# Kernel tuning notes

Hardware: AMD Instinct MI355X
Metric: run time of the kernel (lower is better)

## Reference

```python
import jax, jax.numpy as jnp
import numpy as np

IN_F = 4096
OUT_F = 4096
BATCH = 1024

def setup_inputs() -> dict:
    key = jax.random.key(0)
    k = jax.random.split(key, 7)
    x = jax.random.normal(k[0], (BATCH, IN_F), dtype=jnp.float32)
    weight_mu = jax.random.normal(k[1], (OUT_F, IN_F), dtype=jnp.float32) * (1.0 / np.sqrt(IN_F))
    # torch init: uniform(-5,-3) for sigma params (raw values, used directly as std)
    weight_sigma = jax.random.uniform(k[2], (OUT_F, IN_F), dtype=jnp.float32, minval=-5.0, maxval=-3.0)
    bias_mu = jnp.zeros((OUT_F,), dtype=jnp.float32)
    bias_sigma = jax.random.uniform(k[3], (OUT_F,), dtype=jnp.float32, minval=-5.0, maxval=-3.0)
    eps_w = jax.random.normal(k[4], (OUT_F, IN_F), dtype=jnp.float32)
    eps_b = jax.random.normal(k[5], (OUT_F,), dtype=jnp.float32)
    return {"x": x, "weight_mu": weight_mu, "weight_sigma": weight_sigma,
            "bias_mu": bias_mu, "bias_sigma": bias_sigma,
            "eps_w": eps_w, "eps_b": eps_b}

def reference(x, weight_mu, weight_sigma, bias_mu, bias_sigma, eps_w, eps_b):
    # training-mode forward: reparameterized weight sample then dense matmul
    weight = weight_mu + eps_w * weight_sigma        # [out, in]
    bias = bias_mu + eps_b * bias_sigma              # [out]
    # F.linear(x, W, b) = x @ W.T + b
    return jnp.einsum('bi,oi->bo', x, weight) + bias
```

## Files before the change

### kernel.cpp

```cpp
#include <hip/hip_runtime.h>
#include <hip/hip_bf16.h>
#include <stdint.h>

#define M_BATCH 1024
#define N_OUT   4096
#define K_IN    4096

#define BM 128
#define BN 128
#define BK 64
#define KSPLIT 2
#define KPER  (K_IN / KSPLIT)
#define KITER (KPER / BK)

typedef __attribute__((ext_vector_type(8))) __bf16 bf16x8_t;
typedef __attribute__((ext_vector_type(4))) float f32x4_t;

__device__ __forceinline__ unsigned short f2bf_bits(float f) {
    union { __hip_bfloat16 h; unsigned short u; } cvt;
    cvt.h = __float2bfloat16(f);
    return cvt.u;
}

struct __align__(8) US4 { unsigned short x, y, z, w; };

__global__ __launch_bounds__(256) void prep_kernel(
    const float* __restrict__ x,
    const float* __restrict__ wmu,
    const float* __restrict__ wsig,
    const float* __restrict__ epsw,
    unsigned short* __restrict__ wb,
    unsigned short* __restrict__ xb,
    float4* __restrict__ czero)
{
    const size_t tid    = (size_t)blockIdx.x * blockDim.x + threadIdx.x;
    const size_t stride = (size_t)gridDim.x * blockDim.x;

    const size_t NW4 = (size_t)N_OUT * K_IN / 4;
    const float4* wmu4  = (const float4*)wmu;
    const float4* wsig4 = (const float4*)wsig;
    const float4* epsw4 = (const float4*)epsw;
    US4* wb4 = (US4*)wb;
    for (size_t i = tid; i < NW4; i += stride) {
        float4 m = wmu4[i], s = wsig4[i], e = epsw4[i];
        US4 o;
        o.x = f2bf_bits(fmaf(e.x, s.x, m.x));
        o.y = f2bf_bits(fmaf(e.y, s.y, m.y));
        o.z = f2bf_bits(fmaf(e.z, s.z, m.z));
        o.w = f2bf_bits(fmaf(e.w, s.w, m.w));
        wb4[i] = o;
    }

    const size_t NX4 = (size_t)M_BATCH * K_IN / 4;
    const float4* x4 = (const float4*)x;
    US4* xb4 = (US4*)xb;
    for (size_t i = tid; i < NX4; i += stride) {
        float4 v = x4[i];
        US4 o;
        o.x = f2bf_bits(v.x);
        o.y = f2bf_bits(v.y);
        o.z = f2bf_bits(v.z);
        o.w = f2bf_bits(v.w);
        xb4[i] = o;
    }

    const size_t NC4 = (size_t)M_BATCH * N_OUT / 4;
    const float4 z = {0.f, 0.f, 0.f, 0.f};
    for (size_t i = tid; i < NC4; i += stride) czero[i] = z;
}

__global__ __launch_bounds__(256, 2) void gemm_bt_kernel(
    const unsigned short* __restrict__ A,
    const unsigned short* __restrict__ B,
    const float* __restrict__ bmu,
    const float* __restrict__ bsig,
    const float* __restrict__ ebias,
    float* __restrict__ C)
{
    __shared__ unsigned short As[2 * BM * BK];
    __shared__ unsigned short Bs[2 * BN * BK];

    const int t     = threadIdx.x;
    const int bm0   = blockIdx.y * BM;
    const int bn0   = blockIdx.x * BN;
    const int kbase = blockIdx.z * KPER;
    const int lane  = t & 63;
    const int wave  = t >> 6;
    const int wrow  = (wave >> 1) * 64;
    const int wcol  = (wave & 1) * 64;
    const int lm    = lane & 15;
    const int quad  = lane >> 4;

    f32x4_t acc[4][4] = {};

    const int srow = t >> 3;
    const int jg   = (t & 7) ^ (srow & 7);
    const unsigned short* ag = A + (size_t)(bm0 + srow) * K_IN + kbase + jg * 8;
    const unsigned short* bg = B + (size_t)(bn0 + srow) * K_IN + kbase + jg * 8;
    char* asDst = (char*)As + t * 16;
    char* bsDst = (char*)Bs + t * 16;

    #pragma unroll
    for (int s = 0; s < 4; ++s) {
        __builtin_amdgcn_global_load_lds(
            (const __attribute__((address_space(1))) void*)(ag + (size_t)s * 32 * K_IN),
            (__attribute__((address_space(3))) void*)(asDst + s * 4096), 16, 0, 0);
        __builtin_amdgcn_global_load_lds(
            (const __attribute__((address_space(1))) void*)(bg + (size_t)s * 32 * K_IN),
            (__attribute__((address_space(3))) void*)(bsDst + s * 4096), 16, 0, 0);
    }

    for (int it = 0; it < KITER; ++it) {
        __syncthreads();

        if (it + 1 < KITER) {
            const int koff = (it + 1) * BK;
            const int nb   = ((it + 1) & 1) * 16384;
            #pragma unroll
            for (int s = 0; s < 4; ++s) {
                __builtin_amdgcn_global_load_lds(
                    (const __attribute__((address_space(1))) void*)(ag + (size_t)s * 32 * K_IN + koff),
                    (__attribute__((address_space(3))) void*)(asDst + nb + s * 4096), 16, 0, 0);
                __builtin_amdgcn_global_load_lds(
                    (const __attribute__((address_space(1))) void*)(bg + (size_t)s * 32 * K_IN + koff),
                    (__attribute__((address_space(3))) void*)(bsDst + nb + s * 4096), 16, 0, 0);
            }
        }

        const unsigned short* Ab = As + (it & 1) * 8192;
        const unsigned short* Bb = Bs + (it & 1) * 8192;

        #pragma unroll
        for (int kk = 0; kk < 2; ++kk) {
            const int pbase = kk * 4;
            bf16x8_t a_frag[4], b_frag[4];
            #pragma unroll
            for (int im = 0; im < 4; im++) {
                const int R = wrow + im * 16 + lm;
                const int p = (pbase + quad) ^ (lm & 7);
                a_frag[im] = *(const bf16x8_t*)(Ab + R * BK + p * 8);
            }
            #pragma unroll
            for (int jn = 0; jn < 4; jn++) {
                const int R = wcol + jn * 16 + lm;
                const int p = (pbase + quad) ^ (lm & 7);
                b_frag[jn] = *(const bf16x8_t*)(Bb + R * BK + p * 8);
            }
            #pragma unroll
            for (int im = 0; im < 4; im++)
                #pragma unroll
                for (int jn = 0; jn < 4; jn++)
                    acc[im][jn] = __builtin_amdgcn_mfma_f32_16x16x32_bf16(
                        a_frag[im], b_frag[jn], acc[im][jn], 0, 0, 0);
        }
    }

    #pragma unroll
    for (int jn = 0; jn < 4; jn++) {
        const int gn = bn0 + wcol + jn * 16 + lm;
        const float bias = (kbase == 0) ? (bmu[gn] + ebias[gn] * bsig[gn]) : 0.f;
        #pragma unroll
        for (int im = 0; im < 4; im++) {
            const int gm0 = bm0 + wrow + im * 16 + quad * 4;
            #pragma unroll
            for (int r = 0; r < 4; r++)
                atomicAdd(&C[(size_t)(gm0 + r) * N_OUT + gn], acc[im][jn][r] + bias);
        }
    }
}

__global__ __launch_bounds__(256) void naive_kernel(
    const float* __restrict__ x, const float* __restrict__ wmu,
    const float* __restrict__ wsig, const float* __restrict__ bmu,
    const float* __restrict__ bsig, const float* __restrict__ epsw,
    const float* __restrict__ epsb, float* __restrict__ out)
{
    const int o = blockIdx.x * blockDim.x + threadIdx.x;
    const int b = blockIdx.y;
    const float4* xr = (const float4*)(x + (size_t)b * K_IN);
    const float4* mr = (const float4*)(wmu + (size_t)o * K_IN);
    const float4* sr = (const float4*)(wsig + (size_t)o * K_IN);
    const float4* er = (const float4*)(epsw + (size_t)o * K_IN);
    float s = 0.f;
    for (int k = 0; k < K_IN / 4; k++) {
        float4 xv = xr[k], m = mr[k], sg = sr[k], e = er[k];
        s += xv.x * fmaf(e.x, sg.x, m.x);
        s += xv.y * fmaf(e.y, sg.y, m.y);
        s += xv.z * fmaf(e.z, sg.z, m.z);
        s += xv.w * fmaf(e.w, sg.w, m.w);
    }
    out[(size_t)b * N_OUT + o] = s + bmu[o] + epsb[o] * bsig[o];
}

extern "C" void kernel_launch(void* const* d_in, const int* in_sizes, int n_in,
                              void* d_out, int out_size, void* d_ws, size_t ws_size,
                              hipStream_t stream)
{
    const float* x    = (const float*)d_in[0];
    const float* wmu  = (const float*)d_in[1];
    const float* wsig = (const float*)d_in[2];
    const float* bmu  = (const float*)d_in[3];
    const float* bsig = (const float*)d_in[4];
    const float* epsw = (const float*)d_in[5];
    const float* epsb = (const float*)d_in[6];
    float* out = (float*)d_out;

    const size_t need = ((size_t)N_OUT * K_IN + (size_t)M_BATCH * K_IN) * sizeof(unsigned short);
    if (ws_size >= need) {
        unsigned short* wb = (unsigned short*)d_ws;
        unsigned short* xb = wb + (size_t)N_OUT * K_IN;
        prep_kernel<<<2048, 256, 0, stream>>>(x, wmu, wsig, epsw, wb, xb, (float4*)out);
        dim3 grid(N_OUT / BN, M_BATCH / BM, KSPLIT);
        gemm_bt_kernel<<<grid, 256, 0, stream>>>(xb, wb, bmu, bsig, epsb, out);
    } else {
        dim3 grid(N_OUT / 256, M_BATCH);
        naive_kernel<<<grid, 256, 0, stream>>>(x, wmu, wsig, bmu, bsig, epsw, epsb, out);
    }
}
```

Baseline: 281.1 us.

## Replace split-K atomics with in-block K-split reduction and unrolled prep

The split-K over two blocks with atomicAdd into a pre-zeroed output becomes a single 512-thread block whose two wave groups each handle half of K. The halves are reduced through LDS and written with plain stores plus bias. This removes the output zeroing pass and the global atomics. The prep kernel is also rewritten with a fixed grid, 4-way unrolled nontemporal loads and no grid-stride loop. LDS use doubles to 128KB per block, which likely limits occupancy to one block per CU despite the launch bound of 2.

Measured after the change: 242.7 us. 1.16x faster.

```diff
diff --git a/kernel.cpp b/kernel.cpp
--- a/kernel.cpp
+++ b/kernel.cpp
@@ -9,12 +9,12 @@
 #define BM 128
 #define BN 128
 #define BK 64
-#define KSPLIT 2
-#define KPER  (K_IN / KSPLIT)
+#define KPER  (K_IN / 2)
 #define KITER (KPER / BK)
 
 typedef __attribute__((ext_vector_type(8))) __bf16 bf16x8_t;
 typedef __attribute__((ext_vector_type(4))) float f32x4_t;
+typedef __attribute__((ext_vector_type(4))) float fvec4;
 
 __device__ __forceinline__ unsigned short f2bf_bits(float f) {
     union { __hip_bfloat16 h; unsigned short u; } cvt;
@@ -30,46 +30,44 @@
     const float* __restrict__ wsig,
     const float* __restrict__ epsw,
     unsigned short* __restrict__ wb,
-    unsigned short* __restrict__ xb,
-    float4* __restrict__ czero)
-{
-    const size_t tid    = (size_t)blockIdx.x * blockDim.x + threadIdx.x;
-    const size_t stride = (size_t)gridDim.x * blockDim.x;
-
-    const size_t NW4 = (size_t)N_OUT * K_IN / 4;
-    const float4* wmu4  = (const float4*)wmu;
-    const float4* wsig4 = (const float4*)wsig;
-    const float4* epsw4 = (const float4*)epsw;
+    unsigned short* __restrict__ xb)
+{
+    const size_t tid = (size_t)blockIdx.x * blockDim.x + threadIdx.x;
+    const size_t T   = (size_t)1048576;
+
+    const fvec4* wmu4  = (const fvec4*)wmu;
+    const fvec4* wsig4 = (const fvec4*)wsig;
+    const fvec4* epsw4 = (const fvec4*)epsw;
     US4* wb4 = (US4*)wb;
-    for (size_t i = tid; i < NW4; i += stride) {
-        float4 m = wmu4[i], s = wsig4[i], e = epsw4[i];
+
+    fvec4 m[4], s[4], e[4];
+    #pragma unroll
+    for (int r = 0; r < 4; ++r) {
+        const size_t i = tid + (size_t)r * T;
+        m[r] = __builtin_nontemporal_load(wmu4  + i);
+        s[r] = __builtin_nontemporal_load(wsig4 + i);
+        e[r] = __builtin_nontemporal_load(epsw4 + i);
+    }
+    #pragma unroll
+    for (int r = 0; r < 4; ++r) {
         US4 o;
-        o.x = f2bf_bits(fmaf(e.x, s.x, m.x));
-        o.y = f2bf_bits(fmaf(e.y, s.y, m.y));
-        o.z = f2bf_bits(fmaf(e.z, s.z, m.z));
-        o.w = f2bf_bits(fmaf(e.w, s.w, m.w));
-        wb4[i] = o;
-    }
-
-    const size_t NX4 = (size_t)M_BATCH * K_IN / 4;
-    const float4* x4 = (const float4*)x;
-    US4* xb4 = (US4*)xb;
-    for (size_t i = tid; i < NX4; i += stride) {
-        float4 v = x4[i];
-        US4 o;
-        o.x = f2bf_bits(v.x);
-        o.y = f2bf_bits(v.y);
-        o.z = f2bf_bits(v.z);
-        o.w = f2bf_bits(v.w);
-        xb4[i] = o;
-    }
-
-    const size_t NC4 = (size_t)M_BATCH * N_OUT / 4;
-    const float4 z = {0.f, 0.f, 0.f, 0.f};
-    for (size_t i = tid; i < NC4; i += stride) czero[i] = z;
-}
-
-__global__ __launch_bounds__(256, 2) void gemm_bt_kernel(
+        o.x = f2bf_bits(fmaf(e[r].x, s[r].x, m[r].x));
+        o.y = f2bf_bits(fmaf(e[r].y, s[r].y, m[r].y));
+        o.z = f2bf_bits(fmaf(e[r].z, s[r].z, m[r].z));
+        o.w = f2bf_bits(fmaf(e[r].w, s[r].w, m[r].w));
+        wb4[tid + (size_t)r * T] = o;
+    }
+
+    fvec4 v = __builtin_nontemporal_load((const fvec4*)x + tid);
+    US4 o;
+    o.x = f2bf_bits(v.x);
+    o.y = f2bf_bits(v.y);
+    o.z = f2bf_bits(v.z);
+    o.w = f2bf_bits(v.w);
+    ((US4*)xb)[tid] = o;
+}
+
+__global__ __launch_bounds__(512, 2) void gemm_bt_kernel(
     const unsigned short* __restrict__ A,
     const unsigned short* __restrict__ B,
     const float* __restrict__ bmu,
@@ -77,75 +75,69 @@
     const float* __restrict__ ebias,
     float* __restrict__ C)
 {
-    __shared__ unsigned short As[2 * BM * BK];
-    __shared__ unsigned short Bs[2 * BN * BK];
+    __shared__ unsigned short lds[2 * 32768];
 
     const int t     = threadIdx.x;
     const int bm0   = blockIdx.y * BM;
     const int bn0   = blockIdx.x * BN;
-    const int kbase = blockIdx.z * KPER;
     const int lane  = t & 63;
     const int wave  = t >> 6;
-    const int wrow  = (wave >> 1) * 64;
-    const int wcol  = (wave & 1) * 64;
+    const int khalf = wave >> 2;
+    const int quadw = wave & 3;
+    const int wrow  = (quadw >> 1) * 64;
+    const int wcol  = (quadw & 1) * 64;
     const int lm    = lane & 15;
     const int quad  = lane >> 4;
 
     f32x4_t acc[4][4] = {};
 
-    const int srow = t >> 3;
-    const int jg   = (t & 7) ^ (srow & 7);
-    const unsigned short* ag = A + (size_t)(bm0 + srow) * K_IN + kbase + jg * 8;
-    const unsigned short* bg = B + (size_t)(bn0 + srow) * K_IN + kbase + jg * 8;
-    char* asDst = (char*)As + t * 16;
-    char* bsDst = (char*)Bs + t * 16;
-
-    #pragma unroll
-    for (int s = 0; s < 4; ++s) {
+    const unsigned short* srcs[8];
+    const int rlow = t >> 3;
+    const int jsw  = ((t & 7) ^ (rlow & 7)) * 8;
+    #pragma unroll
+    for (int s = 0; s < 8; ++s) {
+        const int row  = rlow + (s & 1) * 64;
+        const int half = (s >> 1) & 1;
+        const unsigned short* base = (s < 4)
+            ? (A + (size_t)(bm0 + row) * K_IN)
+            : (B + (size_t)(bn0 + row) * K_IN);
+        srcs[s] = base + half * KPER + jsw;
+    }
+    char* dst0 = (char*)lds + t * 16;
+
+    #pragma unroll
+    for (int s = 0; s < 8; ++s)
         __builtin_amdgcn_global_load_lds(
-            (const __attribute__((address_space(1))) void*)(ag + (size_t)s * 32 * K_IN),
-            (__attribute__((address_space(3))) void*)(asDst + s * 4096), 16, 0, 0);
-        __builtin_amdgcn_global_load_lds(
-            (const __attribute__((address_space(1))) void*)(bg + (size_t)s * 32 * K_IN),
-            (__attribute__((address_space(3))) void*)(bsDst + s * 4096), 16, 0, 0);
-    }
+            (const __attribute__((address_space(1))) void*)(srcs[s]),
+            (__attribute__((address_space(3))) void*)(dst0 + s * 8192), 16, 0, 0);
 
     for (int it = 0; it < KITER; ++it) {
         __syncthreads();
 
         if (it + 1 < KITER) {
             const int koff = (it + 1) * BK;
-            const int nb   = ((it + 1) & 1) * 16384;
-            #pragma unroll
-            for (int s = 0; s < 4; ++s) {
+            const int nb   = ((it + 1) & 1) * 65536;
+            #pragma unroll
+            for (int s = 0; s < 8; ++s)
                 __builtin_amdgcn_global_load_lds(
-                    (const __attribute__((address_space(1))) void*)(ag + (size_t)s * 32 * K_IN + koff),
-                    (__attribute__((address_space(3))) void*)(asDst + nb + s * 4096), 16, 0, 0);
-                __builtin_amdgcn_global_load_lds(
-                    (const __attribute__((address_space(1))) void*)(bg + (size_t)s * 32 * K_IN + koff),
-                    (__attribute__((address_space(3))) void*)(bsDst + nb + s * 4096), 16, 0, 0);
-            }
+                    (const __attribute__((address_space(1))) void*)(srcs[s] + koff),
+                    (__attribute__((address_space(3))) void*)(dst0 + nb + s * 8192), 16, 0, 0);
         }
 
-        const unsigned short* Ab = As + (it & 1) * 8192;
-        const unsigned short* Bb = Bs + (it & 1) * 8192;
+        const unsigned short* Lb = lds + (it & 1) * 32768;
+        const unsigned short* Ah = Lb + khalf * 8192;
+        const unsigned short* Bh = Lb + 16384 + khalf * 8192;
 
         #pragma unroll
         for (int kk = 0; kk < 2; ++kk) {
-            const int pbase = kk * 4;
+            const int p = ((kk * 4) + quad) ^ (lm & 7);
             bf16x8_t a_frag[4], b_frag[4];
             #pragma unroll
-            for (int im = 0; im < 4; im++) {
-                const int R = wrow + im * 16 + lm;
-                const int p = (pbase + quad) ^ (lm & 7);
-                a_frag[im] = *(const bf16x8_t*)(Ab + R * BK + p * 8);
-            }
-            #pragma unroll
-            for (int jn = 0; jn < 4; jn++) {
-                const int R = wcol + jn * 16 + lm;
-                const int p = (pbase + quad) ^ (lm & 7);
-                b_frag[jn] = *(const bf16x8_t*)(Bb + R * BK + p * 8);
-            }
+            for (int im = 0; im < 4; im++)
+                a_frag[im] = *(const bf16x8_t*)(Ah + ((wrow + im * 16 + lm) * 8 + p) * 8);
+            #pragma unroll
+            for (int jn = 0; jn < 4; jn++)
+                b_frag[jn] = *(const bf16x8_t*)(Bh + ((wcol + jn * 16 + lm) * 8 + p) * 8);
             #pragma unroll
             for (int im = 0; im < 4; im++)
                 #pragma unroll
@@ -155,16 +147,28 @@
         }
     }
 
-    #pragma unroll
-    for (int jn = 0; jn < 4; jn++) {
-        const int gn = bn0 + wcol + jn * 16 + lm;
-        const float bias = (kbase == 0) ? (bmu[gn] + ebias[gn] * bsig[gn]) : 0.f;
+    f32x4_t* red = (f32x4_t*)lds;
+    if (wave >= 4) {
         #pragma unroll
-        for (int im = 0; im < 4; im++) {
-            const int gm0 = bm0 + wrow + im * 16 + quad * 4;
-            #pragma unroll
-            for (int r = 0; r < 4; r++)
-                atomicAdd(&C[(size_t)(gm0 + r) * N_OUT + gn], acc[im][jn][r] + bias);
+        for (int im = 0; im < 4; im++)
+            #pragma unroll
+            for (int jn = 0; jn < 4; jn++)
+                red[quadw * 1024 + (im * 4 + jn) * 64 + lane] = acc[im][jn];
+    }
+    __syncthreads();
+    if (wave < 4) {
+        #pragma unroll
+        for (int jn = 0; jn < 4; jn++) {
+            const int gn = bn0 + wcol + jn * 16 + lm;
+            const float bias = bmu[gn] + ebias[gn] * bsig[gn];
+            #pragma unroll
+            for (int im = 0; im < 4; im++) {
+                const f32x4_t part = red[quadw * 1024 + (im * 4 + jn) * 64 + lane];
+                const int gm0 = bm0 + wrow + im * 16 + quad * 4;
+                #pragma unroll
+                for (int r = 0; r < 4; r++)
+                    C[(size_t)(gm0 + r) * N_OUT + gn] = acc[im][jn][r] + part[r] + bias;
+            }
         }
     }
 }
@@ -209,9 +213,9 @@
     if (ws_size >= need) {
         unsigned short* wb = (unsigned short*)d_ws;
         unsigned short* xb = wb + (size_t)N_OUT * K_IN;
-        prep_kernel<<<2048, 256, 0, stream>>>(x, wmu, wsig, epsw, wb, xb, (float4*)out);
-        dim3 grid(N_OUT / BN, M_BATCH / BM, KSPLIT);
-        gemm_bt_kernel<<<grid, 256, 0, stream>>>(xb, wb, bmu, bsig, epsb, out);
+        prep_kernel<<<4096, 256, 0, stream>>>(x, wmu, wsig, epsw, wb, xb);
+        dim3 grid(N_OUT / BN, M_BATCH / BM);
+        gemm_bt_kernel<<<grid, 512, 0, stream>>>(xb, wb, bmu, bsig, epsb, out);
     } else {
         dim3 grid(N_OUT / 256, M_BATCH);
         naive_kernel<<<grid, 256, 0, stream>>>(x, wmu, wsig, bmu, bsig, epsw, epsb, out);
```
